# Kernel tuning notes

Hardware: AMD Instinct MI355X
Metric: run time of the kernel (lower is better)

## Reference

```python
import jax, jax.numpy as jnp
import numpy as np

CUTOFF = 5.0
BOX = 15.0
SPECIES = [1, 6, 8]
N_NODES = 10000
N_EDGES = 200000
ETAS = [0.01, 0.05, 0.1]
ZETAS = [1.0, 2.0, 4.0, 8.0]
LAMBDAS = [-1.0, 1.0]


def _cartesian_params():
    # matches torch.cartesian_prod(etas, zetas, lambdas): etas outermost
    e, zt, lb = np.meshgrid(np.float32(ETAS), np.float32(ZETAS), np.float32(LAMBDAS), indexing='ij')
    return e.ravel(), zt.ravel(), lb.ravel()  # each [24]


def _build_triplets(rng):
    # edges: edge_index[0]=j (source), edge_index[1]=i (target)
    j = rng.integers(0, N_NODES, N_EDGES)
    i = rng.integers(0, N_NODES, N_EDGES)
    edge_shift = rng.integers(-1, 2, (N_EDGES, 3)).astype(np.float32)
    # CSR of adj_t (row=i, col=j): for edge e, triplet partners k are cols of row j[e]
    order = np.argsort(i, kind='stable')
    cols = j[order]
    cnt = np.bincount(i, minlength=N_NODES)
    rowptr = np.concatenate([[0], np.cumsum(cnt)])
    num_trip = cnt[j]
    T = int(num_trip.sum())
    e_of_t = np.repeat(np.arange(N_EDGES), num_trip)
    starts = np.repeat(np.cumsum(num_trip) - num_trip, num_trip)
    local = np.arange(T) - starts
    idx_k = cols[rowptr[j[e_of_t]] + local]
    idx_i = i[e_of_t]
    idx_j = j[e_of_t]
    shift_t = edge_shift[e_of_t]
    m = idx_i != idx_k
    return idx_i[m], idx_j[m], idx_k[m], shift_t[m]


def setup_inputs() -> dict:
    rng = np.random.default_rng(0)
    pos = rng.uniform(0.0, BOX, (N_NODES, 3)).astype(np.float32)
    cell = (np.eye(3, dtype=np.float32) * BOX)[None]  # [1,3,3]
    z = np.asarray(SPECIES, dtype=np.int64)[rng.integers(0, 3, N_NODES)]
    batch = np.zeros(N_NODES, dtype=np.int64)
    idx_i, idx_j, idx_k, edge_shift_i = _build_triplets(rng)
    etas, zetas, lambdas = _cartesian_params()
    return {
        'pos': jnp.asarray(pos), 'cell': jnp.asarray(cell),
        'z': jnp.asarray(z), 'batch': jnp.asarray(batch),
        'idx_i': jnp.asarray(idx_i), 'idx_j': jnp.asarray(idx_j), 'idx_k': jnp.asarray(idx_k),
        'edge_shift_i': jnp.asarray(edge_shift_i),
        'etas': jnp.asarray(etas), 'zetas': jnp.asarray(zetas), 'lambdas': jnp.asarray(lambdas),
    }


def _cutoff_fn(r):
    return 0.5 * (jnp.cos(jnp.pi * r / CUTOFF) + 1.0) * (r < CUTOFF).astype(r.dtype)


def reference(pos, cell, z, batch, idx_i, idx_j, idx_k, edge_shift_i, etas, zetas, lambdas):
    n_nodes = pos.shape[0]
    pos_i = pos[idx_i]                       # [T,3]
    cell_t = cell[batch[idx_i]]              # [T,3,3]
    shift = jnp.einsum('ni,nij->nj', edge_shift_i, cell_t)
    vec_ij = pos[idx_j] - pos_i + shift
    vec_ik = pos[idx_k] - pos_i + shift
    r_ij = jnp.linalg.norm(vec_ij, axis=-1)
    r_ik = jnp.linalg.norm(vec_ik, axis=-1)
    r_jk = jnp.linalg.norm(vec_ik - vec_ij, axis=-1)
    cos_ijk = jnp.sum(vec_ij * vec_ik, axis=-1) / (r_ij * r_ik + 1e-12)

    # [P,T] angular descriptor; base (1 + lambda*cos) >= 0 since lambda = +/-1
    G4 = (jnp.power(2.0, 1.0 - zetas)[:, None]
          * jnp.power(1.0 + lambdas[:, None] * cos_ijk[None, :], zetas[:, None])
          * jnp.exp(-etas[:, None] * (r_ij**2 + r_ik**2 + r_jk**2)[None, :] / CUTOFF**2)
          * (_cutoff_fn(r_ij) * _cutoff_fn(r_ik) * _cutoff_fn(r_jk))[None, :])

    zj = z[idx_j]
    zk = z[idx_k]
    outs = []
    for sp in SPECIES:
        mask = ((zj == sp) & (zk == sp)).astype(G4.dtype)
        outs.append(jax.ops.segment_sum((G4 * mask).T, idx_i, num_segments=n_nodes).T / 2)
    pairs = [(SPECIES[a], SPECIES[b]) for a in range(len(SPECIES)) for b in range(a + 1, len(SPECIES))]
    for sp_j, sp_k in pairs:
        mask = (((zj == sp_j) & (zk == sp_k)) | ((zj == sp_k) & (zk == sp_j))).astype(G4.dtype)
        outs.append(jax.ops.segment_sum((G4 * mask).T, idx_i, num_segments=n_nodes).T / 2)
    return jnp.concatenate(outs, axis=0)  # [6*P, N]
```

## Files before the change

### kernel.cpp

```cpp
#include <hip/hip_runtime.h>
#include <math.h>

#define CUTOFF_R  5.0f
#define CUT2      25.0f
#define INV_CUT2  (1.0f / 25.0f)
#define PI_OVER_CUT (3.14159265358979323846f / CUTOFF_R)
#define NPARAM 24

__device__ __noinline__ void rare_accumulate(
    int i, int j, int k,
    float vjx, float vjy, float vjz,
    float vkx, float vky, float vkz,
    float r2ij, float r2ik, float r2jk,
    const int* __restrict__ z,
    const float* __restrict__ etas,
    float* __restrict__ out, int N)
{
    float rij = sqrtf(r2ij);
    float rik = sqrtf(r2ik);
    float rjk = sqrtf(r2jk);

    float fc = 0.125f * (cosf(PI_OVER_CUT * rij) + 1.0f)
                      * (cosf(PI_OVER_CUT * rik) + 1.0f)
                      * (cosf(PI_OVER_CUT * rjk) + 1.0f);

    float cos_ijk = (vjx * vkx + vjy * vky + vjz * vkz) / (rij * rik + 1e-12f);
    float ssum = (r2ij + r2ik + r2jk) * INV_CUT2;

    int zj = z[j], zk = z[k];
    int a = (zj == 1) ? 0 : ((zj == 6) ? 1 : 2);
    int c = (zk == 1) ? 0 : ((zk == 6) ? 1 : 2);
    int ch = (a == c) ? a : (2 + a + c);

    float* obase = out + (size_t)ch * NPARAM * N + i;
    float fch = 0.5f * fc;

    float bm = 1.0f - cos_ijk;
    float bp = 1.0f + cos_ijk;
    float pw[4][2];
    pw[0][0] = bm;                 pw[0][1] = bp;
    pw[1][0] = bm * bm;            pw[1][1] = bp * bp;
    pw[2][0] = pw[1][0]*pw[1][0];  pw[2][1] = pw[1][1]*pw[1][1];
    pw[3][0] = pw[2][0]*pw[2][0];  pw[3][1] = pw[2][1]*pw[2][1];
    const float coef[4] = {1.0f, 0.5f, 0.125f, 0.0078125f};

    #pragma unroll
    for (int e = 0; e < 3; ++e) {
        float ee = expf(-etas[e * 8] * ssum) * fch;
        #pragma unroll
        for (int zi = 0; zi < 4; ++zi) {
            float cz = coef[zi] * ee;
            atomicAdd(obase + (size_t)(e * 8 + zi * 2 + 0) * N, cz * pw[zi][0]);
            atomicAdd(obase + (size_t)(e * 8 + zi * 2 + 1) * N, cz * pw[zi][1]);
        }
    }
}

__global__ void pad_pos_kernel(const float* __restrict__ pos,
                               float4* __restrict__ pos4, int N)
{
    int u = blockIdx.x * blockDim.x + threadIdx.x;
    if (u < N)
        pos4[u] = make_float4(pos[3*u], pos[3*u+1], pos[3*u+2], 0.0f);
}

__global__ __launch_bounds__(256) void g4_kernel(
    const float4* __restrict__ pos4,
    const float* __restrict__ cell,
    const int*   __restrict__ z,
    const int*   __restrict__ idx_i,
    const int*   __restrict__ idx_j,
    const int*   __restrict__ idx_k,
    const float* __restrict__ shift,
    const float* __restrict__ etas,
    float* __restrict__ out,
    int T, int N)
{
    int t = blockIdx.x * blockDim.x + threadIdx.x;
    if (t >= T) return;

    float C00 = cell[0], C01 = cell[1], C02 = cell[2];
    float C10 = cell[3], C11 = cell[4], C12 = cell[5];
    float C20 = cell[6], C21 = cell[7], C22 = cell[8];

    int i = idx_i[t];
    int j = idx_j[t];
    int k = idx_k[t];
    float s0 = shift[3*t+0];
    float s1 = shift[3*t+1];
    float s2 = shift[3*t+2];

    float4 pi = pos4[i];
    float4 pj = pos4[j];

    float shx = s0 * C00 + s1 * C10 + s2 * C20;
    float shy = s0 * C01 + s1 * C11 + s2 * C21;
    float shz = s0 * C02 + s1 * C12 + s2 * C22;

    float ox = shx - pi.x, oy = shy - pi.y, oz = shz - pi.z;
    float vjx = pj.x + ox, vjy = pj.y + oy, vjz = pj.z + oz;
    float r2ij = vjx*vjx + vjy*vjy + vjz*vjz;

    if (r2ij >= CUT2) return;
    float4 pk = pos4[k];
    float vkx = pk.x + ox, vky = pk.y + oy, vkz = pk.z + oz;
    float r2ik = vkx*vkx + vky*vky + vkz*vkz;
    float dx = vkx - vjx, dy = vky - vjy, dz = vkz - vjz;
    float r2jk = dx*dx + dy*dy + dz*dz;

    if ((r2ik < CUT2) & (r2jk < CUT2)) {
        rare_accumulate(i, j, k, vjx, vjy, vjz, vkx, vky, vkz,
                        r2ij, r2ik, r2jk, z, etas, out, N);
    }
}

extern "C" void kernel_launch(void* const* d_in, const int* in_sizes, int n_in,
                              void* d_out, int out_size, void* d_ws, size_t ws_size,
                              hipStream_t stream) {
    const float* pos     = (const float*)d_in[0];
    const float* cell    = (const float*)d_in[1];
    const int*   z       = (const int*)d_in[2];
    const int*   idx_i   = (const int*)d_in[4];
    const int*   idx_j   = (const int*)d_in[5];
    const int*   idx_k   = (const int*)d_in[6];
    const float* shift   = (const float*)d_in[7];
    const float* etas    = (const float*)d_in[8];
    float* out = (float*)d_out;

    int T = in_sizes[4];
    int N = in_sizes[0] / 3;

    float4* pos4 = (float4*)d_ws;

    hipMemsetAsync(d_out, 0, (size_t)out_size * sizeof(float), stream);
    pad_pos_kernel<<<(N + 255) / 256, 256, 0, stream>>>(pos, pos4, N);

    int block = 256;
    int grid = (T + block - 1) / block;
    g4_kernel<<<grid, block, 0, stream>>>(pos4, cell, z,
                                          idx_i, idx_j, idx_k, shift,
                                          etas, out, T, N);
}
```

Baseline: 138.0 us.

## Split triplet processing into stream-compaction filter and compacted accumulation pass

```diff
diff --git a/kernel.cpp b/kernel.cpp
--- a/kernel.cpp
+++ b/kernel.cpp
@@ -1,116 +1,151 @@
 #include <hip/hip_runtime.h>
 #include <math.h>
 
-#define CUTOFF_R  5.0f
 #define CUT2      25.0f
 #define INV_CUT2  (1.0f / 25.0f)
-#define PI_OVER_CUT (3.14159265358979323846f / CUTOFF_R)
+#define PI_OVER_CUT (3.14159265358979323846f / 5.0f)
 #define NPARAM 24
 
-__device__ __noinline__ void rare_accumulate(
-    int i, int j, int k,
-    float vjx, float vjy, float vjz,
-    float vkx, float vky, float vkz,
-    float r2ij, float r2ik, float r2jk,
-    const int* __restrict__ z,
-    const float* __restrict__ etas,
-    float* __restrict__ out, int N)
-{
-    float rij = sqrtf(r2ij);
-    float rik = sqrtf(r2ik);
-    float rjk = sqrtf(r2jk);
-
-    float fc = 0.125f * (cosf(PI_OVER_CUT * rij) + 1.0f)
-                      * (cosf(PI_OVER_CUT * rik) + 1.0f)
-                      * (cosf(PI_OVER_CUT * rjk) + 1.0f);
-
-    float cos_ijk = (vjx * vkx + vjy * vky + vjz * vkz) / (rij * rik + 1e-12f);
-    float ssum = (r2ij + r2ik + r2jk) * INV_CUT2;
-
-    int zj = z[j], zk = z[k];
-    int a = (zj == 1) ? 0 : ((zj == 6) ? 1 : 2);
-    int c = (zk == 1) ? 0 : ((zk == 6) ? 1 : 2);
-    int ch = (a == c) ? a : (2 + a + c);
-
-    float* obase = out + (size_t)ch * NPARAM * N + i;
-    float fch = 0.5f * fc;
-
-    float bm = 1.0f - cos_ijk;
-    float bp = 1.0f + cos_ijk;
-    float pw[4][2];
-    pw[0][0] = bm;                 pw[0][1] = bp;
-    pw[1][0] = bm * bm;            pw[1][1] = bp * bp;
-    pw[2][0] = pw[1][0]*pw[1][0];  pw[2][1] = pw[1][1]*pw[1][1];
-    pw[3][0] = pw[2][0]*pw[2][0];  pw[3][1] = pw[2][1]*pw[2][1];
-    const float coef[4] = {1.0f, 0.5f, 0.125f, 0.0078125f};
-
-    #pragma unroll
-    for (int e = 0; e < 3; ++e) {
-        float ee = expf(-etas[e * 8] * ssum) * fch;
-        #pragma unroll
-        for (int zi = 0; zi < 4; ++zi) {
-            float cz = coef[zi] * ee;
-            atomicAdd(obase + (size_t)(e * 8 + zi * 2 + 0) * N, cz * pw[zi][0]);
-            atomicAdd(obase + (size_t)(e * 8 + zi * 2 + 1) * N, cz * pw[zi][1]);
-        }
-    }
-}
-
-__global__ void pad_pos_kernel(const float* __restrict__ pos,
-                               float4* __restrict__ pos4, int N)
+__global__ void prep_kernel(const float* __restrict__ pos,
+                            float4* __restrict__ pos4,
+                            int* __restrict__ counter, int N)
 {
     int u = blockIdx.x * blockDim.x + threadIdx.x;
+    if (u == 0) *counter = 0;
     if (u < N)
         pos4[u] = make_float4(pos[3*u], pos[3*u+1], pos[3*u+2], 0.0f);
 }
 
-__global__ __launch_bounds__(256) void g4_kernel(
+__global__ __launch_bounds__(256) void filter_kernel(
     const float4* __restrict__ pos4,
     const float* __restrict__ cell,
-    const int*   __restrict__ z,
-    const int*   __restrict__ idx_i,
-    const int*   __restrict__ idx_j,
-    const int*   __restrict__ idx_k,
+    const int* __restrict__ idx_i,
+    const int* __restrict__ idx_j,
+    const float* __restrict__ shift,
+    int* __restrict__ counter,
+    int* __restrict__ tlist,
+    int T)
+{
+    int t = blockIdx.x * blockDim.x + threadIdx.x;
+    bool alive = false;
+    if (t < T) {
+        float C00 = cell[0], C01 = cell[1], C02 = cell[2];
+        float C10 = cell[3], C11 = cell[4], C12 = cell[5];
+        float C20 = cell[6], C21 = cell[7], C22 = cell[8];
+
+        int i = idx_i[t];
+        int j = idx_j[t];
+        float s0 = shift[3*t+0], s1 = shift[3*t+1], s2 = shift[3*t+2];
+
+        float4 pi = pos4[i];
+        float4 pj = pos4[j];
+
+        float shx = s0 * C00 + s1 * C10 + s2 * C20;
+        float shy = s0 * C01 + s1 * C11 + s2 * C21;
+        float shz = s0 * C02 + s1 * C12 + s2 * C22;
+
+        float vjx = pj.x - pi.x + shx;
+        float vjy = pj.y - pi.y + shy;
+        float vjz = pj.z - pi.z + shz;
+        float r2ij = vjx*vjx + vjy*vjy + vjz*vjz;
+        alive = (r2ij < CUT2);
+    }
+
+    unsigned long long m = __ballot(alive);
+    if (m == 0ull) return;
+    int lane   = threadIdx.x & 63;
+    int leader = __ffsll((unsigned long long)m) - 1;
+    int base = 0;
+    if (lane == leader) base = atomicAdd(counter, __popcll(m));
+    base = __shfl(base, leader, 64);
+    if (alive) {
+        int off = __popcll(m & ((1ull << lane) - 1ull));
+        tlist[base + off] = t;
+    }
+}
+
+__global__ __launch_bounds__(256) void accum_kernel(
+    const float4* __restrict__ pos4,
+    const float* __restrict__ cell,
+    const int* __restrict__ z,
+    const int* __restrict__ idx_i,
+    const int* __restrict__ idx_j,
+    const int* __restrict__ idx_k,
     const float* __restrict__ shift,
     const float* __restrict__ etas,
+    const int* __restrict__ counter,
+    const int* __restrict__ tlist,
     float* __restrict__ out,
-    int T, int N)
+    int N)
 {
-    int t = blockIdx.x * blockDim.x + threadIdx.x;
-    if (t >= T) return;
-
+    int total = *counter;
     float C00 = cell[0], C01 = cell[1], C02 = cell[2];
     float C10 = cell[3], C11 = cell[4], C12 = cell[5];
     float C20 = cell[6], C21 = cell[7], C22 = cell[8];
 
-    int i = idx_i[t];
-    int j = idx_j[t];
-    int k = idx_k[t];
-    float s0 = shift[3*t+0];
-    float s1 = shift[3*t+1];
-    float s2 = shift[3*t+2];
+    int stride = gridDim.x * blockDim.x;
+    for (int u = blockIdx.x * blockDim.x + threadIdx.x; u < total; u += stride) {
+        int t = tlist[u];
+        int i = idx_i[t], j = idx_j[t], k = idx_k[t];
+        float s0 = shift[3*t+0], s1 = shift[3*t+1], s2 = shift[3*t+2];
 
-    float4 pi = pos4[i];
-    float4 pj = pos4[j];
+        float4 pi = pos4[i];
+        float4 pj = pos4[j];
+        float4 pk = pos4[k];
 
-    float shx = s0 * C00 + s1 * C10 + s2 * C20;
-    float shy = s0 * C01 + s1 * C11 + s2 * C21;
-    float shz = s0 * C02 + s1 * C12 + s2 * C22;
+        float shx = s0 * C00 + s1 * C10 + s2 * C20;
+        float shy = s0 * C01 + s1 * C11 + s2 * C21;
+        float shz = s0 * C02 + s1 * C12 + s2 * C22;
 
-    float ox = shx - pi.x, oy = shy - pi.y, oz = shz - pi.z;
-    float vjx = pj.x + ox, vjy = pj.y + oy, vjz = pj.z + oz;
-    float r2ij = vjx*vjx + vjy*vjy + vjz*vjz;
+        float ox = shx - pi.x, oy = shy - pi.y, oz = shz - pi.z;
+        float vjx = pj.x + ox, vjy = pj.y + oy, vjz = pj.z + oz;
+        float vkx = pk.x + ox, vky = pk.y + oy, vkz = pk.z + oz;
 
-    if (r2ij >= CUT2) return;
-    float4 pk = pos4[k];
-    float vkx = pk.x + ox, vky = pk.y + oy, vkz = pk.z + oz;
-    float r2ik = vkx*vkx + vky*vky + vkz*vkz;
-    float dx = vkx - vjx, dy = vky - vjy, dz = vkz - vjz;
-    float r2jk = dx*dx + dy*dy + dz*dz;
+        float r2ij = vjx*vjx + vjy*vjy + vjz*vjz;
+        float r2ik = vkx*vkx + vky*vky + vkz*vkz;
+        float dx = vkx - vjx, dy = vky - vjy, dz = vkz - vjz;
+        float r2jk = dx*dx + dy*dy + dz*dz;
 
-    if ((r2ik < CUT2) & (r2jk < CUT2)) {
-        rare_accumulate(i, j, k, vjx, vjy, vjz, vkx, vky, vkz,
-                        r2ij, r2ik, r2jk, z, etas, out, N);
+        if ((r2ik >= CUT2) | (r2jk >= CUT2)) continue;
+
+        float rij = sqrtf(r2ij);
+        float rik = sqrtf(r2ik);
+        float rjk = sqrtf(r2jk);
+
+        float fc = 0.125f * (cosf(PI_OVER_CUT * rij) + 1.0f)
+                          * (cosf(PI_OVER_CUT * rik) + 1.0f)
+                          * (cosf(PI_OVER_CUT * rjk) + 1.0f);
+
+        float cos_ijk = (vjx * vkx + vjy * vky + vjz * vkz) / (rij * rik + 1e-12f);
+        float ssum = (r2ij + r2ik + r2jk) * INV_CUT2;
+
+        int zj = z[j], zk = z[k];
+        int a = (zj == 1) ? 0 : ((zj == 6) ? 1 : 2);
+        int c = (zk == 1) ? 0 : ((zk == 6) ? 1 : 2);
+        int ch = (a == c) ? a : (2 + a + c);
+
+        float* obase = out + (size_t)ch * NPARAM * N + i;
+        float fch = 0.5f * fc;
+
+        float bm = 1.0f - cos_ijk;
+        float bp = 1.0f + cos_ijk;
+        float pw[4][2];
+        pw[0][0] = bm;                 pw[0][1] = bp;
+        pw[1][0] = bm * bm;            pw[1][1] = bp * bp;
+        pw[2][0] = pw[1][0]*pw[1][0];  pw[2][1] = pw[1][1]*pw[1][1];
+        pw[3][0] = pw[2][0]*pw[2][0];  pw[3][1] = pw[2][1]*pw[2][1];
+        const float coef[4] = {1.0f, 0.5f, 0.125f, 0.0078125f};
+
+        #pragma unroll
+        for (int e = 0; e < 3; ++e) {
+            float ee = expf(-etas[e * 8] * ssum) * fch;
+            #pragma unroll
+            for (int zi = 0; zi < 4; ++zi) {
+                float cz = coef[zi] * ee;
+                atomicAdd(obase + (size_t)(e * 8 + zi * 2 + 0) * N, cz * pw[zi][0]);
+                atomicAdd(obase + (size_t)(e * 8 + zi * 2 + 1) * N, cz * pw[zi][1]);
+            }
+        }
     }
 }
 
@@ -130,14 +165,20 @@
     int T = in_sizes[4];
     int N = in_sizes[0] / 3;
 
-    float4* pos4 = (float4*)d_ws;
+    int*    counter = (int*)d_ws;
+    float4* pos4    = (float4*)((char*)d_ws + 256);
+    size_t  pos_bytes = (size_t)16 * N;
+    int*    tlist   = (int*)((char*)d_ws + 256 + ((pos_bytes + 255) & ~(size_t)255));
 
     hipMemsetAsync(d_out, 0, (size_t)out_size * sizeof(float), stream);
-    pad_pos_kernel<<<(N + 255) / 256, 256, 0, stream>>>(pos, pos4, N);
+    prep_kernel<<<(N + 255) / 256, 256, 0, stream>>>(pos, pos4, counter, N);
 
     int block = 256;
-    int grid = (T + block - 1) / block;
-    g4_kernel<<<grid, block, 0, stream>>>(pos4, cell, z,
-                                          idx_i, idx_j, idx_k, shift,
-                                          etas, out, T, N);
+    int grid1 = (T + block - 1) / block;
+    filter_kernel<<<grid1, block, 0, stream>>>(pos4, cell, idx_i, idx_j, shift,
+                                               counter, tlist, T);
+
+    accum_kernel<<<256, block, 0, stream>>>(pos4, cell, z,
+                                            idx_i, idx_j, idx_k, shift, etas,
+                                            counter, tlist, out, N);
 }
```

After: 147.5 us. 1.07x slower.
